# Kernel optimization log

Hardware: AMD Instinct MI355X
Metric: run time of the kernel (lower is better)

The kernel has to match this reference:

```python
import jax, jax.numpy as jnp
import numpy as np

B, S, HID = 4, 2048, 768
H, DBLK, HD = 12, 256, 64  # heads, block_dim = HID//3, head_dim


def setup_inputs() -> dict:
    key = jax.random.key(0)
    ks = jax.random.split(key, 7)
    scale = 0.02
    return {
        "inputs": jax.random.normal(ks[0], (B, S, HID), jnp.float32),
        "Wq": jax.random.normal(ks[1], (H, DBLK, HD), jnp.float32) * scale,
        "bq": jax.random.normal(ks[2], (H, HD), jnp.float32) * scale,
        "Wk": jax.random.normal(ks[3], (H, DBLK, HD), jnp.float32) * scale,
        "bk": jax.random.normal(ks[4], (H, HD), jnp.float32) * scale,
        "Wv": jax.random.normal(ks[5], (H, DBLK, HD), jnp.float32) * scale,
        "bv": jax.random.normal(ks[6], (H, HD), jnp.float32) * scale,
    }


def reference(inputs, Wq, bq, Wk, bk, Wv, bv):
    b, s, hid = inputs.shape
    h, dblk, hd = Wq.shape
    hpm = h // 3  # heads per modality
    # split hidden into 3 modality blocks: [B, S, 3, DBLK]
    xm = inputs.reshape(b, s, 3, dblk)

    def proj(W, bias):
        # block-diagonal GEMM: each modality's x projected by its hpm heads
        y = jnp.einsum('bsmd,mhde->bmhse', xm, W.reshape(3, hpm, dblk, hd))
        y = y + bias.reshape(3, hpm, 1, hd)
        return y.reshape(b, h, s, hd)

    Q = proj(Wq, bq)
    K = proj(Wk, bk)
    V = proj(Wv, bv)

    scores = jnp.einsum('bhse,bhte->bhst', Q, K) / jnp.sqrt(jnp.float32(hd))
    probs = jax.nn.softmax(scores, axis=-1)  # dropout p=0 -> identity
    ctx = jnp.einsum('bhst,bhte->bhse', probs, V)
    # concat heads along feature dim: [B, S, H*HD]
    return ctx.transpose(0, 2, 1, 3).reshape(b, s, h * hd)
```

## Files before the change

kernel.cpp:

```cpp
#include <hip/hip_runtime.h>
#include <hip/hip_bf16.h>

#define B_    4
#define S_    2048
#define HID_  768
#define H_    12
#define DBLK_ 256
#define HD_   64
#define BH_   (B_ * H_)
#define QSZ_  (B_ * H_ * S_ * HD_)
#define WTSZ_ (3 * H_ * HD_ * DBLK_)

typedef _Float16 f16x4 __attribute__((ext_vector_type(4)));
typedef _Float16 f16x8 __attribute__((ext_vector_type(8)));
typedef float    f32x4 __attribute__((ext_vector_type(4)));

#if __has_builtin(__builtin_amdgcn_exp2f)
#define EXP2(x) __builtin_amdgcn_exp2f(x)
#else
#define EXP2(x) exp2f(x)
#endif

typedef const void __attribute__((address_space(1)))* gptr_t;
typedef       void __attribute__((address_space(3)))* sptr_t;

__global__ __launch_bounds__(256) void wconv(
    const float* __restrict__ Wq, const float* __restrict__ Wk,
    const float* __restrict__ Wv, _Float16* __restrict__ whf)
{
    const int idx  = blockIdx.x * 256 + threadIdx.x;
    const int j    = idx & 7;
    const int lane = (idx >> 3) & 63;
    const int et   = (idx >> 9) & 1;
    const int kk   = (idx >> 10) & 7;
    const int eh   = (idx >> 13) & 1;
    const int ph   = idx >> 14;
    const int h    = ph % H_;
    const int p    = ph / H_;
    const int e = eh * 32 + et * 16 + (lane & 15);
    const int k = kk * 32 + (lane >> 4) * 8 + j;
    const float* W = (p == 0) ? Wq : (p == 1) ? Wk : Wv;
    whf[idx] = (_Float16)W[((size_t)h * DBLK_ + k) * HD_ + e];
}

__global__ __launch_bounds__(256, 3) void qkv_proj(
    const float* __restrict__ x, const _Float16* __restrict__ whf,
    const float* __restrict__ bq, const float* __restrict__ bk,
    const float* __restrict__ bv,
    _Float16* __restrict__ qo, _Float16* __restrict__ khf,
    _Float16* __restrict__ vtf)
{
    const int i   = blockIdx.x;
    const int g   = i >> 7;
    const int sc  = i & 127;
    const int m   = g >> 1;
    const int s0g = sc * 64;

    const int tid  = threadIdx.x;
    const int lane = tid & 63;
    const int w    = tid >> 6;
    const int ln   = lane & 15;
    const int qd   = lane >> 4;
    const int h    = 2 * g + (w >> 1);
    const int eh   = w & 1;

    __shared__ _Float16 xs[64 * 256];

    {
        const int rr   = tid >> 6;
        const int c4   = tid & 63;
        const int g16  = c4 >> 1;
        const int half = c4 & 1;
        #pragma unroll
        for (int pass = 0; pass < 16; pass++) {
            const int r = pass * 4 + rr;
            const float4 v = *(const float4*)(
                x + (size_t)(s0g + r) * HID_ + m * DBLK_ + c4 * 4);
            f16x4 hv;
            hv[0] = (_Float16)v.x; hv[1] = (_Float16)v.y;
            hv[2] = (_Float16)v.z; hv[3] = (_Float16)v.w;
            *(f16x4*)(xs + r * 256 + ((g16 ^ (r & 7)) * 8) + half * 4) = hv;
        }
    }
    __syncthreads();

    f32x4 acc[3][2][4];
    #pragma unroll
    for (int p = 0; p < 3; p++)
        #pragma unroll
        for (int et = 0; et < 2; et++)
            #pragma unroll
            for (int st = 0; st < 4; st++)
                acc[p][et][st] = (f32x4){0.f, 0.f, 0.f, 0.f};

    const _Float16* wb = whf + (size_t)((h * 2 + eh) * 16) * 512 + lane * 8;

    for (int kk = 0; kk < 8; kk++) {
        f16x8 a[4];
        #pragma unroll
        for (int st = 0; st < 4; st++)
            a[st] = *(const f16x8*)(
                xs + (st * 16 + ln) * 256 + (((kk * 4 + qd) ^ (ln & 7)) * 8));
        #pragma unroll
        for (int p = 0; p < 3; p++)
            #pragma unroll
            for (int et = 0; et < 2; et++) {
                const f16x8 bb = *(const f16x8*)(
                    wb + (size_t)p * 196608 + (kk * 2 + et) * 512);
                #pragma unroll
                for (int st = 0; st < 4; st++)
                    acc[p][et][st] = __builtin_amdgcn_mfma_f32_16x16x32_f16(
                        a[st], bb, acc[p][et][st], 0, 0, 0);
            }
    }

    const float QS = 0.18033688011112042f;
    const int b    = s0g >> 11;
    const int s0   = s0g & 2047;
    const int bhh  = b * H_ + h;
    const int tile = s0 >> 6;
    const int ht   = w >> 1;

    __syncthreads();
    {
        _Float16* qtile = xs + ht * 4096;
        _Float16* ktile = xs + 8192 + ht * 4096;
        const size_t tbv = (size_t)(bhh * 32 + tile) * 4096;
        #pragma unroll
        for (int et = 0; et < 2; et++) {
            const int d  = eh * 32 + et * 16 + ln;
            const int dc = d >> 3, d7 = d & 7;
            const float biasq = bq[h * HD_ + d];
            const float biask = bk[h * HD_ + d];
            const float biasv = bv[h * HD_ + d];
            #pragma unroll
            for (int st = 0; st < 4; st++) {
                f16x4 vv;
                #pragma unroll
                for (int r = 0; r < 4; r++) vv[r] = (_Float16)(acc[2][et][st][r] + biasv);
                const int vc = st * 2 + (qd >> 1);
                *(f16x4*)(vtf + tbv + d * 64 + ((vc ^ d7) * 8) + (qd & 1) * 4) = vv;
                #pragma unroll
                for (int r = 0; r < 4; r++) {
                    const int sl  = st * 16 + qd * 4 + r;
                    const int rho = (st >> 1) * 32 + (qd & 1) * 16
                                  + ((st & 1) * 2 + (qd >> 1)) * 4 + r;
                    qtile[sl  * 64 + ((dc ^ (sl  & 7)) * 8) + d7] =
                        (_Float16)((acc[0][et][st][r] + biasq) * QS);
                    ktile[rho * 64 + ((dc ^ (rho & 7)) * 8) + d7] =
                        (_Float16)(acc[1][et][st][r] + biask);
                }
            }
        }
    }
    __syncthreads();
    #pragma unroll
    for (int it = 0; it < 4; it++) {
        const int idx  = it * 256 + tid;
        const int ht2  = idx >> 9;
        const int rest = idx & 511;
        const int row  = rest >> 3;
        const int c    = rest & 7;
        const int bhh2 = b * H_ + 2 * g + ht2;
        const f16x8 qv = *(const f16x8*)(xs + ht2 * 4096 + row * 64 + ((c ^ (row & 7)) * 8));
        *(f16x8*)(qo + ((size_t)bhh2 * S_ + s0 + row) * HD_ + c * 8) = qv;
        const f16x8 kv8 = *(const f16x8*)(xs + 8192 + ht2 * 4096 + row * 64 + c * 8);
        *(f16x8*)(khf + (size_t)(bhh2 * 32 + tile) * 4096 + row * 64 + c * 8) = kv8;
    }
}

__global__ __launch_bounds__(256, 3) void attn(
    const _Float16* __restrict__ qh, const _Float16* __restrict__ khf,
    const _Float16* __restrict__ vtf, float* __restrict__ out)
{
    const int i    = blockIdx.x;
    const int slot = i >> 3;
    const int bh   = (i & 7) * 6 + (slot % 6);
    const int qt   = slot / 6;
    const int h = bh % H_, b = bh / H_;
    const int q0 = qt * 128;

    const int tid  = threadIdx.x;
    const int lane = tid & 63;
    const int w    = tid >> 6;
    const int ln   = lane & 15;
    const int qd   = lane >> 4;

    __shared__ __align__(16) char lds[2][16384];

    f16x8 qf[2][2];
    #pragma unroll
    for (int st = 0; st < 2; st++) {
        const _Float16* qb = qh + ((size_t)bh * S_ + q0 + w * 32 + st * 16 + ln) * HD_;
        qf[st][0] = *(const f16x8*)(qb + qd * 8);
        qf[st][1] = *(const f16x8*)(qb + 32 + qd * 8);
    }

    f16x8 ones;
    #pragma unroll
    for (int j = 0; j < 8; j++) ones[j] = (_Float16)1.f;

    f32x4 o[2][4];
    f32x4 lacc[2];
    #pragma unroll
    for (int st = 0; st < 2; st++) {
        lacc[st] = (f32x4){0.f, 0.f, 0.f, 0.f};
        #pragma unroll
        for (int dn = 0; dn < 4; dn++) o[st][dn] = (f32x4){0.f, 0.f, 0.f, 0.f};
    }

    const char* kbase = (const char*)(khf + (size_t)bh * 32 * 4096);
    const char* vbase = (const char*)(vtf + (size_t)bh * 32 * 4096);
    const int   seg   = w * 1024 + lane * 16;
    const int   wseg  = w * 1024;

    auto dma = [&](int it, int buf) {
        const char* ks = kbase + (size_t)it * 8192;
        const char* vs = vbase + (size_t)it * 8192;
        char* lk = &lds[buf][0];
        char* lv = &lds[buf][8192];
        #pragma unroll
        for (int q = 0; q < 2; q++) {
            __builtin_amdgcn_global_load_lds(
                (gptr_t)(ks + q * 4096 + seg), (sptr_t)(lk + q * 4096 + wseg), 16, 0, 0);
            __builtin_amdgcn_global_load_lds(
                (gptr_t)(vs + q * 4096 + seg), (sptr_t)(lv + q * 4096 + wseg), 16, 0, 0);
        }
    };

    dma(0, 0);

    for (int it = 0; it < 32; it++) {
        const int buf = it & 1;
        __syncthreads();
        if (it + 1 < 32) dma(it + 1, buf ^ 1);

        const char* lk = &lds[buf][0];
        const char* lv = &lds[buf][8192];

        f16x8 kf[4][2];
        #pragma unroll
        for (int mt = 0; mt < 4; mt++) {
            kf[mt][0] = *(const f16x8*)(lk + (16 * mt + ln) * 128 + ((qd       ^ (ln & 7)) * 16));
            kf[mt][1] = *(const f16x8*)(lk + (16 * mt + ln) * 128 + (((4 + qd) ^ (ln & 7)) * 16));
        }
        f16x8 vf[4][2];
        #pragma unroll
        for (int dn = 0; dn < 4; dn++)
            #pragma unroll
            for (int p = 0; p < 2; p++)
                vf[dn][p] = *(const f16x8*)(
                    lv + (dn * 16 + ln) * 128 + (((p * 4 + qd) ^ (ln & 7)) * 16));

        #pragma unroll
        for (int st = 0; st < 2; st++) {
            f32x4 s[4];
            #pragma unroll
            for (int mt = 0; mt < 4; mt++) {
                s[mt] = (f32x4){0.f, 0.f, 0.f, 0.f};
                s[mt] = __builtin_amdgcn_mfma_f32_16x16x32_f16(kf[mt][0], qf[st][0], s[mt], 0, 0, 0);
                s[mt] = __builtin_amdgcn_mfma_f32_16x16x32_f16(kf[mt][1], qf[st][1], s[mt], 0, 0, 0);
            }
            #pragma unroll
            for (int p = 0; p < 2; p++) {
                f16x8 a8;
                a8[0] = (_Float16)EXP2(s[2 * p][0]);
                a8[1] = (_Float16)EXP2(s[2 * p][1]);
                a8[2] = (_Float16)EXP2(s[2 * p][2]);
                a8[3] = (_Float16)EXP2(s[2 * p][3]);
                a8[4] = (_Float16)EXP2(s[2 * p + 1][0]);
                a8[5] = (_Float16)EXP2(s[2 * p + 1][1]);
                a8[6] = (_Float16)EXP2(s[2 * p + 1][2]);
                a8[7] = (_Float16)EXP2(s[2 * p + 1][3]);
                lacc[st] = __builtin_amdgcn_mfma_f32_16x16x32_f16(a8, ones, lacc[st], 0, 0, 0);
                #pragma unroll
                for (int dn = 0; dn < 4; dn++)
                    o[st][dn] = __builtin_amdgcn_mfma_f32_16x16x32_f16(
                        a8, vf[dn][p], o[st][dn], 0, 0, 0);
            }
        }
    }

    #pragma unroll
    for (int st = 0; st < 2; st++) {
        float inv[4];
        #pragma unroll
        for (int r = 0; r < 4; r++) inv[r] = 1.f / lacc[st][r];
        #pragma unroll
        for (int dn = 0; dn < 4; dn++) {
            float* op = out + ((size_t)b * S_ + q0 + w * 32 + st * 16 + qd * 4) * HID_
                      + (size_t)h * HD_ + dn * 16 + ln;
            #pragma unroll
            for (int r = 0; r < 4; r++)
                op[(size_t)r * HID_] = o[st][dn][r] * inv[r];
        }
    }
}

extern "C" void kernel_launch(void* const* d_in, const int* in_sizes, int n_in,
                              void* d_out, int out_size, void* d_ws, size_t ws_size,
                              hipStream_t stream) {
    const float* x  = (const float*)d_in[0];
    const float* Wq = (const float*)d_in[1];
    const float* bq = (const float*)d_in[2];
    const float* Wk = (const float*)d_in[3];
    const float* bk = (const float*)d_in[4];
    const float* Wv = (const float*)d_in[5];
    const float* bv = (const float*)d_in[6];
    float* out = (float*)d_out;

    _Float16* q  = (_Float16*)d_ws;
    _Float16* k  = q + QSZ_;
    _Float16* vt = k + QSZ_;
    const size_t need = ((size_t)3 * QSZ_ + WTSZ_) * sizeof(_Float16);
    _Float16* wh = (ws_size >= need) ? (vt + QSZ_)
                                     : (_Float16*)d_out;

    wconv<<<WTSZ_ / 256, 256, 0, stream>>>(Wq, Wk, Wv, wh);
    qkv_proj<<<768, 256, 0, stream>>>(x, wh, bq, bk, bv, q, k, vt);
    attn<<<768, 256, 0, stream>>>(q, k, vt, out);
}
```

Measured before the change: 164.1 us.

## Switch attention kernel to 32x32x16 MFMA tiles with VALU row sums

Restructures the attention inner loop to use 32x32x16 f16 MFMA instead of 16x16x32 for both QK^T and PV. The K tile row permutation in the projection kernel changes to match the new operand layout. The softmax denominator is now summed with VALU adds and a cross-half shuffle, replacing the extra MFMA against a ones vector. Normalisation factors are exchanged through LDS in the epilogue. The larger tiles are meant to cut LDS fragment reads and MFMA issue count, at the cost of larger accumulator register use and more VALU work for the sums.

```diff
diff --git a/kernel.cpp b/kernel.cpp
--- a/kernel.cpp
+++ b/kernel.cpp
@@ -14,6 +14,7 @@
 typedef _Float16 f16x4 __attribute__((ext_vector_type(4)));
 typedef _Float16 f16x8 __attribute__((ext_vector_type(8)));
 typedef float    f32x4 __attribute__((ext_vector_type(4)));
+typedef float    f32x16 __attribute__((ext_vector_type(16)));
 
 #if __has_builtin(__builtin_amdgcn_exp2f)
 #define EXP2(x) __builtin_amdgcn_exp2f(x)
@@ -143,8 +144,7 @@
                 #pragma unroll
                 for (int r = 0; r < 4; r++) {
                     const int sl  = st * 16 + qd * 4 + r;
-                    const int rho = (st >> 1) * 32 + (qd & 1) * 16
-                                  + ((st & 1) * 2 + (qd >> 1)) * 4 + r;
+                    const int rho = st * 16 + (qd & 1) * 8 + (qd >> 1) * 4 + r;
                     qtile[sl  * 64 + ((dc ^ (sl  & 7)) * 8) + d7] =
                         (_Float16)((acc[0][et][st][r] + biasq) * QS);
                     ktile[rho * 64 + ((dc ^ (rho & 7)) * 8) + d7] =
@@ -183,31 +183,26 @@
     const int tid  = threadIdx.x;
     const int lane = tid & 63;
     const int w    = tid >> 6;
-    const int ln   = lane & 15;
-    const int qd   = lane >> 4;
+    const int l5   = lane & 31;
+    const int g    = lane >> 5;
+    const int x7   = l5 & 7;
 
     __shared__ __align__(16) char lds[2][16384];
 
-    f16x8 qf[2][2];
+    f16x8 qf[4];
+    {
+        const _Float16* qb = qh + ((size_t)bh * S_ + q0 + w * 32 + l5) * HD_;
+        #pragma unroll
+        for (int kk = 0; kk < 4; kk++)
+            qf[kk] = *(const f16x8*)(qb + kk * 16 + g * 8);
+    }
+
+    f32x16 o[2];
     #pragma unroll
-    for (int st = 0; st < 2; st++) {
-        const _Float16* qb = qh + ((size_t)bh * S_ + q0 + w * 32 + st * 16 + ln) * HD_;
-        qf[st][0] = *(const f16x8*)(qb + qd * 8);
-        qf[st][1] = *(const f16x8*)(qb + 32 + qd * 8);
-    }
-
-    f16x8 ones;
-    #pragma unroll
-    for (int j = 0; j < 8; j++) ones[j] = (_Float16)1.f;
-
-    f32x4 o[2][4];
-    f32x4 lacc[2];
-    #pragma unroll
-    for (int st = 0; st < 2; st++) {
-        lacc[st] = (f32x4){0.f, 0.f, 0.f, 0.f};
-        #pragma unroll
-        for (int dn = 0; dn < 4; dn++) o[st][dn] = (f32x4){0.f, 0.f, 0.f, 0.f};
-    }
+    for (int dt = 0; dt < 2; dt++)
+        #pragma unroll
+        for (int r = 0; r < 16; r++) o[dt][r] = 0.f;
+    float lp[4] = {0.f, 0.f, 0.f, 0.f};
 
     const char* kbase = (const char*)(khf + (size_t)bh * 32 * 4096);
     const char* vbase = (const char*)(vtf + (size_t)bh * 32 * 4096);
@@ -238,62 +233,57 @@
         const char* lk = &lds[buf][0];
         const char* lv = &lds[buf][8192];
 
-        f16x8 kf[4][2];
-        #pragma unroll
-        for (int mt = 0; mt < 4; mt++) {
-            kf[mt][0] = *(const f16x8*)(lk + (16 * mt + ln) * 128 + ((qd       ^ (ln & 7)) * 16));
-            kf[mt][1] = *(const f16x8*)(lk + (16 * mt + ln) * 128 + (((4 + qd) ^ (ln & 7)) * 16));
-        }
-        f16x8 vf[4][2];
-        #pragma unroll
-        for (int dn = 0; dn < 4; dn++)
-            #pragma unroll
-            for (int p = 0; p < 2; p++)
-                vf[dn][p] = *(const f16x8*)(
-                    lv + (dn * 16 + ln) * 128 + (((p * 4 + qd) ^ (ln & 7)) * 16));
-
-        #pragma unroll
-        for (int st = 0; st < 2; st++) {
-            f32x4 s[4];
-            #pragma unroll
-            for (int mt = 0; mt < 4; mt++) {
-                s[mt] = (f32x4){0.f, 0.f, 0.f, 0.f};
-                s[mt] = __builtin_amdgcn_mfma_f32_16x16x32_f16(kf[mt][0], qf[st][0], s[mt], 0, 0, 0);
-                s[mt] = __builtin_amdgcn_mfma_f32_16x16x32_f16(kf[mt][1], qf[st][1], s[mt], 0, 0, 0);
-            }
-            #pragma unroll
-            for (int p = 0; p < 2; p++) {
-                f16x8 a8;
-                a8[0] = (_Float16)EXP2(s[2 * p][0]);
-                a8[1] = (_Float16)EXP2(s[2 * p][1]);
-                a8[2] = (_Float16)EXP2(s[2 * p][2]);
-                a8[3] = (_Float16)EXP2(s[2 * p][3]);
-                a8[4] = (_Float16)EXP2(s[2 * p + 1][0]);
-                a8[5] = (_Float16)EXP2(s[2 * p + 1][1]);
-                a8[6] = (_Float16)EXP2(s[2 * p + 1][2]);
-                a8[7] = (_Float16)EXP2(s[2 * p + 1][3]);
-                lacc[st] = __builtin_amdgcn_mfma_f32_16x16x32_f16(a8, ones, lacc[st], 0, 0, 0);
-                #pragma unroll
-                for (int dn = 0; dn < 4; dn++)
-                    o[st][dn] = __builtin_amdgcn_mfma_f32_16x16x32_f16(
-                        a8, vf[dn][p], o[st][dn], 0, 0, 0);
-            }
-        }
-    }
-
+        f32x16 c[2];
+        #pragma unroll
+        for (int mt = 0; mt < 2; mt++) {
+            #pragma unroll
+            for (int r = 0; r < 16; r++) c[mt][r] = 0.f;
+            #pragma unroll
+            for (int kk = 0; kk < 4; kk++) {
+                const f16x8 kfr = *(const f16x8*)(
+                    lk + (mt * 32 + l5) * 128 + (((kk * 2 + g) ^ x7) * 16));
+                c[mt] = __builtin_amdgcn_mfma_f32_32x32x16_f16(
+                    kfr, qf[kk], c[mt], 0, 0, 0);
+            }
+        }
+
+        f16x8 a[4];
+        #pragma unroll
+        for (int ks = 0; ks < 4; ks++) {
+            float e[8];
+            #pragma unroll
+            for (int j = 0; j < 8; j++) {
+                e[j] = EXP2(c[ks >> 1][(ks & 1) * 8 + j]);
+                a[ks][j] = (_Float16)e[j];
+            }
+            lp[ks] += ((e[0] + e[1]) + (e[2] + e[3]))
+                    + ((e[4] + e[5]) + (e[6] + e[7]));
+        }
+
+        #pragma unroll
+        for (int dt = 0; dt < 2; dt++)
+            #pragma unroll
+            for (int ks = 0; ks < 4; ks++) {
+                const f16x8 vfr = *(const f16x8*)(
+                    lv + (dt * 32 + l5) * 128 + (((ks * 2 + g) ^ x7) * 16));
+                o[dt] = __builtin_amdgcn_mfma_f32_32x32x16_f16(
+                    a[ks], vfr, o[dt], 0, 0, 0);
+            }
+    }
+
+    float lf = (lp[0] + lp[1]) + (lp[2] + lp[3]);
+    lf += __shfl_xor(lf, 32, 64);
+    float* lsc = (float*)(void*)&lds[0][0] + w * 64;
+    lsc[lane] = 1.f / lf;
+    __syncthreads();
     #pragma unroll
-    for (int st = 0; st < 2; st++) {
-        float inv[4];
-        #pragma unroll
-        for (int r = 0; r < 4; r++) inv[r] = 1.f / lacc[st][r];
-        #pragma unroll
-        for (int dn = 0; dn < 4; dn++) {
-            float* op = out + ((size_t)b * S_ + q0 + w * 32 + st * 16 + qd * 4) * HID_
-                      + (size_t)h * HD_ + dn * 16 + ln;
-            #pragma unroll
-            for (int r = 0; r < 4; r++)
-                op[(size_t)r * HID_] = o[st][dn][r] * inv[r];
-        }
+    for (int r = 0; r < 16; r++) {
+        const int qrow = (r & 3) + 8 * (r >> 2) + 4 * g;
+        const float li = lsc[qrow];
+        float* op = out + ((size_t)b * S_ + q0 + w * 32 + qrow) * HID_
+                  + (size_t)h * HD_ + l5;
+        op[0]  = o[0][r] * li;
+        op[32] = o[1][r] * li;
     }
 }
 
```

After: 165.6 us. Within noise of the previous version (+0.9%).

## Software-pipeline QK MFMAs with exp/PV stage across half-tiles

Applied to the files above, without the earlier changes.

Splits each KV tile into two halves and interleaves the QK^T MFMAs of one half with the exp2 and PV MFMAs of the previous half, carrying score registers across loop iterations. The aim is to let MFMA work overlap the transcendental/convert latency and LDS reads instead of running them serially. This costs extra live registers for two score/V fragment sets, which can lower occupancy, and it adds a prologue/epilogue.

```diff
diff --git a/kernel.cpp b/kernel.cpp
--- a/kernel.cpp
+++ b/kernel.cpp
@@ -228,58 +228,73 @@
         }
     };
 
+    f32x4 scA[2][2], scB[2][2];
+    f16x8 vfA[4], vfB[4];
+
+    auto qk_stage = [&](const char* lk, const char* lv, int p,
+                        f32x4 (&scx)[2][2], f16x8 (&vfx)[4]) {
+        f16x8 kf[2][2];
+        #pragma unroll
+        for (int j = 0; j < 2; j++) {
+            const int mt = 2 * p + j;
+            kf[j][0] = *(const f16x8*)(lk + (16 * mt + ln) * 128 + ((qd       ^ (ln & 7)) * 16));
+            kf[j][1] = *(const f16x8*)(lk + (16 * mt + ln) * 128 + (((4 + qd) ^ (ln & 7)) * 16));
+        }
+        #pragma unroll
+        for (int dn = 0; dn < 4; dn++)
+            vfx[dn] = *(const f16x8*)(
+                lv + (dn * 16 + ln) * 128 + (((p * 4 + qd) ^ (ln & 7)) * 16));
+        #pragma unroll
+        for (int st = 0; st < 2; st++)
+            #pragma unroll
+            for (int j = 0; j < 2; j++) {
+                f32x4 s = (f32x4){0.f, 0.f, 0.f, 0.f};
+                s = __builtin_amdgcn_mfma_f32_16x16x32_f16(kf[j][0], qf[st][0], s, 0, 0, 0);
+                s = __builtin_amdgcn_mfma_f32_16x16x32_f16(kf[j][1], qf[st][1], s, 0, 0, 0);
+                scx[st][j] = s;
+            }
+    };
+
+    auto finish_stage = [&](const f32x4 (&scx)[2][2], const f16x8 (&vfx)[4]) {
+        #pragma unroll
+        for (int st = 0; st < 2; st++) {
+            f16x8 a8;
+            a8[0] = (_Float16)EXP2(scx[st][0][0]);
+            a8[1] = (_Float16)EXP2(scx[st][0][1]);
+            a8[2] = (_Float16)EXP2(scx[st][0][2]);
+            a8[3] = (_Float16)EXP2(scx[st][0][3]);
+            a8[4] = (_Float16)EXP2(scx[st][1][0]);
+            a8[5] = (_Float16)EXP2(scx[st][1][1]);
+            a8[6] = (_Float16)EXP2(scx[st][1][2]);
+            a8[7] = (_Float16)EXP2(scx[st][1][3]);
+            lacc[st] = __builtin_amdgcn_mfma_f32_16x16x32_f16(a8, ones, lacc[st], 0, 0, 0);
+            #pragma unroll
+            for (int dn = 0; dn < 4; dn++)
+                o[st][dn] = __builtin_amdgcn_mfma_f32_16x16x32_f16(
+                    a8, vfx[dn], o[st][dn], 0, 0, 0);
+        }
+    };
+
     dma(0, 0);
 
-    for (int it = 0; it < 32; it++) {
-        const int buf = it & 1;
+    __syncthreads();
+    dma(1, 1);
+    qk_stage(&lds[0][0], &lds[0][8192], 0, scA, vfA);
+    qk_stage(&lds[0][0], &lds[0][8192], 1, scB, vfB);
+    finish_stage(scA, vfA);
+
+    for (int t = 1; t < 32; ++t) {
+        const int buf = t & 1;
         __syncthreads();
-        if (it + 1 < 32) dma(it + 1, buf ^ 1);
-
+        if (t + 1 < 32) dma(t + 1, (t + 1) & 1);
         const char* lk = &lds[buf][0];
         const char* lv = &lds[buf][8192];
-
-        f16x8 kf[4][2];
-        #pragma unroll
-        for (int mt = 0; mt < 4; mt++) {
-            kf[mt][0] = *(const f16x8*)(lk + (16 * mt + ln) * 128 + ((qd       ^ (ln & 7)) * 16));
-            kf[mt][1] = *(const f16x8*)(lk + (16 * mt + ln) * 128 + (((4 + qd) ^ (ln & 7)) * 16));
-        }
-        f16x8 vf[4][2];
-        #pragma unroll
-        for (int dn = 0; dn < 4; dn++)
-            #pragma unroll
-            for (int p = 0; p < 2; p++)
-                vf[dn][p] = *(const f16x8*)(
-                    lv + (dn * 16 + ln) * 128 + (((p * 4 + qd) ^ (ln & 7)) * 16));
-
-        #pragma unroll
-        for (int st = 0; st < 2; st++) {
-            f32x4 s[4];
-            #pragma unroll
-            for (int mt = 0; mt < 4; mt++) {
-                s[mt] = (f32x4){0.f, 0.f, 0.f, 0.f};
-                s[mt] = __builtin_amdgcn_mfma_f32_16x16x32_f16(kf[mt][0], qf[st][0], s[mt], 0, 0, 0);
-                s[mt] = __builtin_amdgcn_mfma_f32_16x16x32_f16(kf[mt][1], qf[st][1], s[mt], 0, 0, 0);
-            }
-            #pragma unroll
-            for (int p = 0; p < 2; p++) {
-                f16x8 a8;
-                a8[0] = (_Float16)EXP2(s[2 * p][0]);
-                a8[1] = (_Float16)EXP2(s[2 * p][1]);
-                a8[2] = (_Float16)EXP2(s[2 * p][2]);
-                a8[3] = (_Float16)EXP2(s[2 * p][3]);
-                a8[4] = (_Float16)EXP2(s[2 * p + 1][0]);
-                a8[5] = (_Float16)EXP2(s[2 * p + 1][1]);
-                a8[6] = (_Float16)EXP2(s[2 * p + 1][2]);
-                a8[7] = (_Float16)EXP2(s[2 * p + 1][3]);
-                lacc[st] = __builtin_amdgcn_mfma_f32_16x16x32_f16(a8, ones, lacc[st], 0, 0, 0);
-                #pragma unroll
-                for (int dn = 0; dn < 4; dn++)
-                    o[st][dn] = __builtin_amdgcn_mfma_f32_16x16x32_f16(
-                        a8, vf[dn][p], o[st][dn], 0, 0, 0);
-            }
-        }
-    }
+        qk_stage(lk, lv, 0, scA, vfA);
+        finish_stage(scB, vfB);
+        qk_stage(lk, lv, 1, scB, vfB);
+        finish_stage(scA, vfA);
+    }
+    finish_stage(scB, vfB);
 
     #pragma unroll
     for (int st = 0; st < 2; st++) {
```

Result: no change. 165.7 us (+0.9%).

## Software-pipeline attention loop with register double-buffered K/V fragments

Applied to the files above, without the earlier changes.

Restructures the main attention loop into a two-stage software pipeline. K/V fragments now live in two register sets, LDS reads for the next tile are issued while QK and softmax-PV MFMAs run on the current tile, and sched_barriers pin the ordering. The goal is to hide LDS read latency and barrier stalls behind matrix work. In exchange it raises VGPR pressure, which may reduce occupancy, and the reordered DMA and sync placement needs care to stay race-free.

```diff
diff --git a/kernel.cpp b/kernel.cpp
--- a/kernel.cpp
+++ b/kernel.cpp
@@ -228,57 +228,78 @@
         }
     };
 
-    dma(0, 0);
-
-    for (int it = 0; it < 32; it++) {
-        const int buf = it & 1;
-        __syncthreads();
-        if (it + 1 < 32) dma(it + 1, buf ^ 1);
-
+    auto rd = [&](int buf, f16x8 (&kf)[4][2], f16x8 (&vf)[4][2]) {
         const char* lk = &lds[buf][0];
         const char* lv = &lds[buf][8192];
-
-        f16x8 kf[4][2];
         #pragma unroll
         for (int mt = 0; mt < 4; mt++) {
             kf[mt][0] = *(const f16x8*)(lk + (16 * mt + ln) * 128 + ((qd       ^ (ln & 7)) * 16));
             kf[mt][1] = *(const f16x8*)(lk + (16 * mt + ln) * 128 + (((4 + qd) ^ (ln & 7)) * 16));
         }
-        f16x8 vf[4][2];
         #pragma unroll
         for (int dn = 0; dn < 4; dn++)
             #pragma unroll
             for (int p = 0; p < 2; p++)
                 vf[dn][p] = *(const f16x8*)(
                     lv + (dn * 16 + ln) * 128 + (((p * 4 + qd) ^ (ln & 7)) * 16));
-
-        #pragma unroll
-        for (int st = 0; st < 2; st++) {
-            f32x4 s[4];
-            #pragma unroll
-            for (int mt = 0; mt < 4; mt++) {
-                s[mt] = (f32x4){0.f, 0.f, 0.f, 0.f};
-                s[mt] = __builtin_amdgcn_mfma_f32_16x16x32_f16(kf[mt][0], qf[st][0], s[mt], 0, 0, 0);
-                s[mt] = __builtin_amdgcn_mfma_f32_16x16x32_f16(kf[mt][1], qf[st][1], s[mt], 0, 0, 0);
-            }
-            #pragma unroll
-            for (int p = 0; p < 2; p++) {
-                f16x8 a8;
-                a8[0] = (_Float16)EXP2(s[2 * p][0]);
-                a8[1] = (_Float16)EXP2(s[2 * p][1]);
-                a8[2] = (_Float16)EXP2(s[2 * p][2]);
-                a8[3] = (_Float16)EXP2(s[2 * p][3]);
-                a8[4] = (_Float16)EXP2(s[2 * p + 1][0]);
-                a8[5] = (_Float16)EXP2(s[2 * p + 1][1]);
-                a8[6] = (_Float16)EXP2(s[2 * p + 1][2]);
-                a8[7] = (_Float16)EXP2(s[2 * p + 1][3]);
-                lacc[st] = __builtin_amdgcn_mfma_f32_16x16x32_f16(a8, ones, lacc[st], 0, 0, 0);
-                #pragma unroll
-                for (int dn = 0; dn < 4; dn++)
-                    o[st][dn] = __builtin_amdgcn_mfma_f32_16x16x32_f16(
-                        a8, vf[dn][p], o[st][dn], 0, 0, 0);
-            }
-        }
+    };
+
+    auto qk = [&](const f16x8 (&kf)[4][2], int st, f32x4 (&s)[4]) {
+        #pragma unroll
+        for (int mt = 0; mt < 4; mt++) {
+            s[mt] = (f32x4){0.f, 0.f, 0.f, 0.f};
+            s[mt] = __builtin_amdgcn_mfma_f32_16x16x32_f16(kf[mt][0], qf[st][0], s[mt], 0, 0, 0);
+            s[mt] = __builtin_amdgcn_mfma_f32_16x16x32_f16(kf[mt][1], qf[st][1], s[mt], 0, 0, 0);
+        }
+    };
+
+    auto smpv = [&](const f32x4 (&s)[4], int st, const f16x8 (&vf)[4][2]) {
+        #pragma unroll
+        for (int p = 0; p < 2; p++) {
+            f16x8 a8;
+            a8[0] = (_Float16)EXP2(s[2 * p][0]);
+            a8[1] = (_Float16)EXP2(s[2 * p][1]);
+            a8[2] = (_Float16)EXP2(s[2 * p][2]);
+            a8[3] = (_Float16)EXP2(s[2 * p][3]);
+            a8[4] = (_Float16)EXP2(s[2 * p + 1][0]);
+            a8[5] = (_Float16)EXP2(s[2 * p + 1][1]);
+            a8[6] = (_Float16)EXP2(s[2 * p + 1][2]);
+            a8[7] = (_Float16)EXP2(s[2 * p + 1][3]);
+            lacc[st] = __builtin_amdgcn_mfma_f32_16x16x32_f16(a8, ones, lacc[st], 0, 0, 0);
+            #pragma unroll
+            for (int dn = 0; dn < 4; dn++)
+                o[st][dn] = __builtin_amdgcn_mfma_f32_16x16x32_f16(
+                    a8, vf[dn][p], o[st][dn], 0, 0, 0);
+        }
+    };
+
+    f16x8 kfA[4][2], vfA[4][2], kfB[4][2], vfB[4][2];
+    f32x4 s0[4], s1[4];
+
+    dma(0, 0);
+    dma(1, 1);
+    __syncthreads();
+    rd(0, kfA, vfA);
+
+    for (int t = 0; t < 32; t += 2) {
+        qk(kfA, 0, s0);
+        __syncthreads();
+        rd(1, kfB, vfB);
+        if (t + 2 < 32) dma(t + 2, 0);
+        qk(kfA, 1, s1);
+        smpv(s0, 0, vfA);
+        smpv(s1, 1, vfA);
+        __builtin_amdgcn_sched_barrier(0);
+        qk(kfB, 0, s0);
+        if (t + 2 < 32) {
+            __syncthreads();
+            rd(0, kfA, vfA);
+            if (t + 3 < 32) dma(t + 3, 1);
+        }
+        qk(kfB, 1, s1);
+        smpv(s0, 0, vfB);
+        smpv(s1, 1, vfB);
+        __builtin_amdgcn_sched_barrier(0);
     }
 
     #pragma unroll
```

Result: slower. 436.6 us (+166.0%).
